# Kernel optimization log

Hardware: AMD Instinct MI355X
Metric: run time of the kernel (lower is better)

Reference implementation:

```python
import jax, jax.numpy as jnp
import numpy as np

N_STEP = 64
GAMMA = 10.0
DIST_MIN, DIST_MAX = 0.0, 10.0
N_LAYER = 4
H_DIM, E_DIM, HID_DIM = 128, 16, 256
N_NODES, N_EDGES = 10000, 320000


def setup_inputs() -> dict:
    key = jax.random.key(0)
    ks = jax.random.split(key, 12)
    in_m = 2 * H_DIM + E_DIM + N_STEP  # 336
    s = 0.02
    return {
        "x": jax.random.normal(ks[0], (N_NODES, H_DIM), jnp.float32),
        "pos": jax.random.normal(ks[1], (N_NODES, 3), jnp.float32),
        "edge_index": jax.random.randint(ks[2], (2, N_EDGES), 0, N_NODES),
        "edge_attr": jax.random.normal(ks[3], (N_EDGES, E_DIM), jnp.float32),
        "Wm": jax.random.normal(ks[4], (N_LAYER, in_m, HID_DIM), jnp.float32) * s,
        "bm": jnp.zeros((N_LAYER, HID_DIM), jnp.float32),
        "Wp": jax.random.normal(ks[5], (N_LAYER, HID_DIM, 1), jnp.float32) * s,
        "bp": jnp.zeros((N_LAYER, 1), jnp.float32),
        "Wx": jax.random.normal(ks[6], (N_LAYER, H_DIM + HID_DIM, H_DIM), jnp.float32) * s,
        "bx": jnp.zeros((N_LAYER, H_DIM), jnp.float32),
    }


def _egnn_layer(x, pos, edge_index, edge_attr, Wm, bm, Wp, bp, Wx, bx):
    i, j = edge_index[0], edge_index[1]
    n = x.shape[0]
    x_i, x_j = x[i], x[j]                       # [E, h] gathers
    # NOTE: source uses x (not pos) for the distance feature -- replicated.
    r = jnp.linalg.norm(x_i - x_j, axis=1)      # [E]
    c = jnp.linspace(DIST_MIN, DIST_MAX, N_STEP, dtype=x.dtype)
    soh = jnp.exp(-GAMMA * (r[:, None] - c[None, :]) ** 2)  # [E, n_step]
    m_ij = jnp.concatenate([x_i, x_j, soh, edge_attr], axis=1) @ Wm + bm  # [E, hid]
    _alpha = m_ij @ Wp + bp  # computed but unused in source's _update_pos
    # position update: scatter-mean of pos_i - pos_j over destination i
    pos_vect = pos[i] - pos[j]                  # [E, 3]
    cnt = jax.ops.segment_sum(jnp.ones((i.shape[0],), pos.dtype), i, num_segments=n)
    pos_aggr = jax.ops.segment_sum(pos_vect, i, num_segments=n) / jnp.maximum(cnt, 1.0)[:, None]
    pos = pos + pos_aggr
    # feature update: scatter-sum of messages
    m_aggr = jax.ops.segment_sum(m_ij, i, num_segments=n)  # [N, hid]
    x = jnp.concatenate([x, m_aggr], axis=1) @ Wx + bx      # [N, h]
    return x, pos


def reference(x, pos, edge_index, edge_attr, Wm, bm, Wp, bp, Wx, bx):
    x_ori = x
    for l in range(N_LAYER):
        x, pos = _egnn_layer(x, pos, edge_index, edge_attr,
                             Wm[l], bm[l], Wp[l], bp[l], Wx[l], bx[l])
        x = jax.nn.leaky_relu(x)
    x = x_ori + x            # residual_connection == 'add'
    x = jax.nn.leaky_relu(x)  # activate_last
    return x, pos
```

## Files before the change

### kernel.cpp

```cpp
#include <hip/hip_runtime.h>
#include <hip/hip_bf16.h>

#define NN 10000
#define NE 320000
#define HD 128
#define ED 16
#define HID 256
#define KP 480
#define AST 488
#define CAP 96
#define NBF 2161

typedef unsigned short ushort_t;
typedef long long i64;
typedef __attribute__((ext_vector_type(8))) short short8;
typedef __attribute__((ext_vector_type(4))) float f32x4;
typedef __attribute__((ext_vector_type(4))) unsigned int u32x4;

__device__ __forceinline__ float leaky(float v){ return v > 0.f ? v : 0.01f*v; }
__device__ __forceinline__ ushort_t f2bs(float v){
  __hip_bfloat16 b = __float2bfloat16(v);
  return *(ushort_t*)&b;
}
__device__ __forceinline__ unsigned pack2u(float a, float b){
  return (unsigned)f2bs(a) | ((unsigned)f2bs(b) << 16);
}
__device__ __forceinline__ float bl(unsigned u){ return __uint_as_float(u << 16); }
__device__ __forceinline__ float bh(unsigned u){ return __uint_as_float(u & 0xffff0000u); }
__device__ __forceinline__ float2 cvt2(unsigned u){ return make_float2(bl(u), bh(u)); }

__global__ __launch_bounds__(256) void k_misc(const float* __restrict__ x, ushort_t* __restrict__ xb,
                                              const int* __restrict__ ii, const int* __restrict__ jj,
                                              int* __restrict__ cnt, i64* __restrict__ sje,
                                              const float* __restrict__ Wx,
                                              const float* __restrict__ Wm, const float* __restrict__ bm,
                                              ushort_t* __restrict__ WcT){
  if (blockIdx.x < NBF){
    int t = blockIdx.x*256 + threadIdx.x;
    const int S1 = NE;
    const int S2 = NE + NN*HD/8;
    if (t < S1){
      int e = t;
      int a  = __builtin_nontemporal_load(ii + e);
      int jv = __builtin_nontemporal_load(jj + e);
      int r = atomicAdd(&cnt[a], 1);
      if (r < CAP)
        sje[(long)a*CAP + r] = ((i64)e << 32) | (unsigned)jv;
    } else if (t < S2){
      int u = t - S1;
      f32x4 a = __builtin_nontemporal_load(((const f32x4*)x) + 2*u);
      f32x4 b = __builtin_nontemporal_load(((const f32x4*)x) + 2*u + 1);
      u32x4 o;
      o.x = pack2u(a.x, a.y); o.y = pack2u(a.z, a.w);
      o.z = pack2u(b.x, b.y); o.w = pack2u(b.z, b.w);
      __builtin_nontemporal_store(o, ((u32x4*)xb) + u);
    } else if (t < S2 + 4*HD*HD){
      int u = t - S2;
      int l = u >> 14, r = (u >> 7) & 127, c = u & 127;
      float w = __builtin_nontemporal_load(Wx + (long)l*(HD+HID)*HD + r*HD + c);
      WcT[((long)l*HD + c)*KP + r] = f2bs(w);
    } else {
      int u = t - S2 - 4*HD*HD;
      if (u < 4*HD*15){
        int row = u / 15, k = 465 + u % 15;
        WcT[(long)row*KP + k] = 0;
      }
    }
    return;
  }
  __shared__ float a_s[16*36];
  __shared__ float w_s[16*128];
  int bi = blockIdx.x - NBF;
  int t  = threadIdx.x;
  int rb = (bi % 11) * 32;
  int l  = bi / 11;
  int lr = t >> 4, lk = t & 15;
  int wcc = t & 127, wk = t >> 7;
  int cg = t & 31, rg = t >> 5;
  const float* Wxb = Wx + (long)l*(HD+HID)*HD + HD*HD;
  float acc[4][4];
  #pragma unroll
  for (int i = 0; i < 4; ++i)
    #pragma unroll
    for (int j = 0; j < 4; ++j) acc[i][j] = 0.f;
  for (int k0 = 0; k0 < HID; k0 += 16){
    int m0 = rb + lr, m1 = rb + lr + 16;
    float v0 = 0.f, v1 = 0.f;
    if (m0 < 336) v0 = Wm[((long)l*336 + m0)*HID + k0 + lk];
    else if (m0 == 336) v0 = bm[l*HID + k0 + lk];
    if (m1 < 336) v1 = Wm[((long)l*336 + m1)*HID + k0 + lk];
    else if (m1 == 336) v1 = bm[l*HID + k0 + lk];
    a_s[lk*36 + lr]      = v0;
    a_s[lk*36 + lr + 16] = v1;
    #pragma unroll
    for (int q = 0; q < 8; ++q)
      w_s[(wk + 2*q)*128 + wcc] = Wxb[(k0 + wk + 2*q)*HD + wcc];
    __syncthreads();
    #pragma unroll
    for (int k = 0; k < 16; ++k){
      float4 av = *(const float4*)&a_s[k*36 + rg*4];
      float4 wv = *(const float4*)&w_s[k*128 + cg*4];
      acc[0][0] += av.x*wv.x; acc[0][1] += av.x*wv.y; acc[0][2] += av.x*wv.z; acc[0][3] += av.x*wv.w;
      acc[1][0] += av.y*wv.x; acc[1][1] += av.y*wv.y; acc[1][2] += av.y*wv.z; acc[1][3] += av.y*wv.w;
      acc[2][0] += av.z*wv.x; acc[2][1] += av.z*wv.y; acc[2][2] += av.z*wv.z; acc[2][3] += av.z*wv.w;
      acc[3][0] += av.w*wv.x; acc[3][1] += av.w*wv.y; acc[3][2] += av.w*wv.z; acc[3][3] += av.w*wv.w;
    }
    __syncthreads();
  }
  #pragma unroll
  for (int i = 0; i < 4; ++i){
    int m = rb + rg*4 + i;
    if (m < 337){
      #pragma unroll
      for (int j = 0; j < 4; ++j)
        WcT[((long)l*HD + cg*4 + j)*KP + 128 + m] = f2bs(acc[i][j]);
    }
  }
}

template<int FIRST, int FINAL>
__global__ __launch_bounds__(256) void k_layer(const uint4* __restrict__ xb4, const float* __restrict__ posf_cur,
                                               const int* __restrict__ cnt, const i64* __restrict__ sje,
                                               const float* __restrict__ ea,
                                               ushort_t* __restrict__ inv,
                                               const ushort_t* __restrict__ WcT, const float* __restrict__ bx,
                                               ushort_t* __restrict__ xb_next, const float* __restrict__ x_ori,
                                               float* __restrict__ out, float* __restrict__ posf_next){
  __shared__ ushort_t Asm[8*AST];
  __shared__ int sjL[8][64];
  __shared__ int seL[FIRST ? 8 : 1][64];
  int tid = threadIdx.x;
  int nl  = tid >> 5;
  int n   = blockIdx.x*8 + nl;
  int sub = tid & 31;
  int g   = sub >> 4;
  int gl  = sub & 15;
  int len = cnt[n];
  long beg = (long)n*CAP;
  int len2 = len < 64 ? len : 64;

  if (sub < len2){
    i64 lv = __builtin_nontemporal_load(sje + beg + sub);
    sjL[nl][sub] = (int)lv;
    if (FIRST) seL[nl][sub] = (int)(lv >> 32);
  }
  if (sub + 32 < len2){
    i64 lv = __builtin_nontemporal_load(sje + beg + sub + 32);
    sjL[nl][sub + 32] = (int)lv;
    if (FIRST) seL[nl][sub + 32] = (int)(lv >> 32);
  }
  __builtin_amdgcn_wave_barrier();

  uint4 xi = xb4[(long)n*16 + gl];
  float2 xi0 = cvt2(xi.x), xi1 = cvt2(xi.y), xi2 = cvt2(xi.z), xi3 = cvt2(xi.w);
  float c0 = (10.0f/63.0f)*(float)(4*gl);
  float c1 = (10.0f/63.0f)*(float)(4*gl+1);
  float c2 = (10.0f/63.0f)*(float)(4*gl+2);
  float c3 = (10.0f/63.0f)*(float)(4*gl+3);

  float2 s0 = {0,0}, s1 = {0,0}, s2 = {0,0}, s3 = {0,0};
  float h0 = 0, h1 = 0, h2 = 0, h3 = 0, sp = 0, sea = 0;
  int ec = gl & 3;
  int es = gl >> 2;

#define DPART(Bv, P) { \
    float2 e0=cvt2(Bv.x), e1=cvt2(Bv.y), e2=cvt2(Bv.z), e3=cvt2(Bv.w); \
    float d, q=0.f; \
    d=xi0.x-e0.x; q+=d*d;  d=xi0.y-e0.y; q+=d*d; \
    d=xi1.x-e1.x; q+=d*d;  d=xi1.y-e1.y; q+=d*d; \
    d=xi2.x-e2.x; q+=d*d;  d=xi2.y-e2.y; q+=d*d; \
    d=xi3.x-e3.x; q+=d*d;  d=xi3.y-e3.y; q+=d*d; \
    s0.x+=e0.x; s0.y+=e0.y; s1.x+=e1.x; s1.y+=e1.y; \
    s2.x+=e2.x; s2.y+=e2.y; s3.x+=e3.x; s3.y+=e3.y; \
    P = q; }

#define HPART(P) { \
    float r = sqrtf(P); \
    float t0=r-c0, t1=r-c1, t2=r-c2, t3=r-c3; \
    h0 += __expf(-10.f*t0*t0); h1 += __expf(-10.f*t1*t1); \
    h2 += __expf(-10.f*t2*t2); h3 += __expf(-10.f*t3*t3); }

#define LOADB(Bx, jx, ex, wv, off) { \
    jx[0]=sjL[nl][(off)]; jx[1]=sjL[nl][(off)+1]; jx[2]=sjL[nl][(off)+2]; jx[3]=sjL[nl][(off)+3]; \
    if (FIRST){ ex[0]=seL[nl][(off)]; ex[1]=seL[nl][(off)+1]; ex[2]=seL[nl][(off)+2]; ex[3]=seL[nl][(off)+3]; } \
    Bx[0] = xb4[(long)jx[0]*16 + gl]; \
    Bx[1] = xb4[(long)jx[1]*16 + gl]; \
    Bx[2] = xb4[(long)jx[2]*16 + gl]; \
    Bx[3] = xb4[(long)jx[3]*16 + gl]; \
    int jsel = (es==0) ? jx[0] : (es==1) ? jx[1] : (es==2) ? jx[2] : jx[3]; \
    wv = 0.f; \
    if (ec < 3) wv = posf_cur[(long)jsel*3 + ec]; }

#define COMPUTE(Bx, jx, ex, wv) { \
    float y0=0,y1=0,y2=0,y3=0; \
    if (FIRST){ \
      y0 = __builtin_nontemporal_load(ea + (long)ex[0]*ED + gl); \
      y1 = __builtin_nontemporal_load(ea + (long)ex[1]*ED + gl); \
      y2 = __builtin_nontemporal_load(ea + (long)ex[2]*ED + gl); \
      y3 = __builtin_nontemporal_load(ea + (long)ex[3]*ED + gl); } \
    float p0_,p1_,p2_,p3_; \
    DPART(Bx[0], p0_) DPART(Bx[1], p1_) DPART(Bx[2], p2_) DPART(Bx[3], p3_) \
    p0_ += __shfl_xor(p0_,1,64); p1_ += __shfl_xor(p1_,1,64); p2_ += __shfl_xor(p2_,1,64); p3_ += __shfl_xor(p3_,1,64); \
    p0_ += __shfl_xor(p0_,2,64); p1_ += __shfl_xor(p1_,2,64); p2_ += __shfl_xor(p2_,2,64); p3_ += __shfl_xor(p3_,2,64); \
    p0_ += __shfl_xor(p0_,4,64); p1_ += __shfl_xor(p1_,4,64); p2_ += __shfl_xor(p2_,4,64); p3_ += __shfl_xor(p3_,4,64); \
    p0_ += __shfl_xor(p0_,8,64); p1_ += __shfl_xor(p1_,8,64); p2_ += __shfl_xor(p2_,8,64); p3_ += __shfl_xor(p3_,8,64); \
    HPART(p0_) HPART(p1_) HPART(p2_) HPART(p3_) \
    sp += wv; \
    if (FIRST) sea += (y0+y1)+(y2+y3); }

#define EP1(Jv, Ev) { \
    uint4 Bv = xb4[(long)(Jv)*16 + gl]; \
    float wv1 = 0; if (gl < 3) wv1 = posf_cur[(long)(Jv)*3 + gl]; \
    float yv = 0; if (FIRST) yv = __builtin_nontemporal_load(ea + (long)(Ev)*ED + gl); \
    float pv; DPART(Bv, pv) \
    pv += __shfl_xor(pv,1,64); pv += __shfl_xor(pv,2,64); \
    pv += __shfl_xor(pv,4,64); pv += __shfl_xor(pv,8,64); \
    HPART(pv) \
    sp += wv1; if (FIRST) sea += yv; }

  int lo   = g ? (len2 >> 1) : 0;
  int hi   = g ? len2 : (len2 >> 1);
  int cntg = hi - lo;
  int nb4  = cntg >> 2;

  uint4 BA[4], BB_[4];
  int jA[4], jB[4], eA[4], eB[4];
  float wA, wB;
  (void)eA; (void)eB;
  if (nb4 > 0){
    LOADB(BA, jA, eA, wA, lo)
    int b = 1;
    for (; b + 1 < nb4; b += 2){
      LOADB(BB_, jB, eB, wB, lo + 4*b)
      COMPUTE(BA, jA, eA, wA)
      LOADB(BA, jA, eA, wA, lo + 4*b + 4)
      COMPUTE(BB_, jB, eB, wB)
    }
    if (b < nb4){
      LOADB(BB_, jB, eB, wB, lo + 4*b)
      COMPUTE(BA, jA, eA, wA)
      COMPUTE(BB_, jB, eB, wB)
    } else {
      COMPUTE(BA, jA, eA, wA)
    }
  }
  for (int k = lo + (nb4 << 2); k < hi; ++k){
    int jv = sjL[nl][k];
    int ev = FIRST ? seL[nl][k] : 0;
    EP1(jv, ev)
  }
  for (int q2 = 64 + g; q2 < len; q2 += 2){
    i64 lv = sje[beg + q2];
    int jv = (int)lv;
    int ev = FIRST ? (int)(lv >> 32) : 0;
    EP1(jv, ev)
  }
#undef DPART
#undef HPART
#undef LOADB
#undef COMPUTE
#undef EP1

  sp += __shfl_xor(sp,4,64); sp += __shfl_xor(sp,8,64);

  s0.x += __shfl_xor(s0.x,16,64); s0.y += __shfl_xor(s0.y,16,64);
  s1.x += __shfl_xor(s1.x,16,64); s1.y += __shfl_xor(s1.y,16,64);
  s2.x += __shfl_xor(s2.x,16,64); s2.y += __shfl_xor(s2.y,16,64);
  s3.x += __shfl_xor(s3.x,16,64); s3.y += __shfl_xor(s3.y,16,64);
  h0 += __shfl_xor(h0,16,64); h1 += __shfl_xor(h1,16,64);
  h2 += __shfl_xor(h2,16,64); h3 += __shfl_xor(h3,16,64);
  sp += __shfl_xor(sp,16,64);
  if (FIRST) sea += __shfl_xor(sea,16,64);

  if (g == 0){
    float cf = (float)len;
    ushort_t* Ar = Asm + nl*AST;
    ((uint4*)Ar)[gl] = xi;
    ((uint4*)(Ar + 128))[gl] = make_uint4(pack2u(cf*xi0.x, cf*xi0.y), pack2u(cf*xi1.x, cf*xi1.y),
                                          pack2u(cf*xi2.x, cf*xi2.y), pack2u(cf*xi3.x, cf*xi3.y));
    ((uint4*)(Ar + 256))[gl] = make_uint4(pack2u(s0.x, s0.y), pack2u(s1.x, s1.y),
                                          pack2u(s2.x, s2.y), pack2u(s3.x, s3.y));
    ((uint2*)(Ar + 384))[gl] = make_uint2(pack2u(h0, h1), pack2u(h2, h3));
    ushort_t sea_us;
    if (FIRST){
      sea_us = f2bs(sea);
      __builtin_nontemporal_store(sea_us, inv + (long)n*16 + gl);
    } else {
      sea_us = __builtin_nontemporal_load(inv + (long)n*16 + gl);
    }
    Ar[448 + gl] = sea_us;
    Ar[464 + gl] = (gl == 0) ? f2bs(cf) : (ushort_t)0;
    if (gl < 3){
      float pi = posf_cur[n*3 + gl];
      posf_next[n*3 + gl] = pi + (cf*pi - sp) / fmaxf(cf, 1.f);
    }
  }
  __syncthreads();

  int wave = tid >> 6, lane = tid & 63;
  int quad = lane >> 4, l16 = lane & 15;
  int nb = wave * 32;
  const ushort_t* Arow = Asm + (l16 & 7)*AST + quad*8;
  const ushort_t* W0 = WcT + (long)(nb + l16)*KP + quad*8;
  const ushort_t* W1 = WcT + (long)(nb + 16 + l16)*KP + quad*8;
  f32x4 acc0 = {0,0,0,0}, acc1 = {0,0,0,0};
  for (int k0 = 0; k0 < KP; k0 += 32){
    short8 av = *(const short8*)(Arow + k0);
    short8 b0 = *(const short8*)(W0 + k0);
    short8 b1 = *(const short8*)(W1 + k0);
    acc0 = __builtin_amdgcn_mfma_f32_16x16x32_bf16(av, b0, acc0, 0, 0, 0);
    acc1 = __builtin_amdgcn_mfma_f32_16x16x32_bf16(av, b1, acc1, 0, 0, 0);
  }
  float bx0 = bx[nb + l16], bx1 = bx[nb + 16 + l16];
  #pragma unroll
  for (int r = 0; r < 4; ++r){
    int row = quad*4 + r;
    if (row < 8){
      long base = (long)(blockIdx.x*8 + row)*HD;
      float v0 = leaky(acc0[r] + bx0);
      float v1 = leaky(acc1[r] + bx1);
      if (FINAL){
        float o0 = __builtin_nontemporal_load(x_ori + base + nb + l16);
        float o1 = __builtin_nontemporal_load(x_ori + base + nb + 16 + l16);
        __builtin_nontemporal_store(leaky(o0 + v0), out + base + nb + l16);
        __builtin_nontemporal_store(leaky(o1 + v1), out + base + nb + 16 + l16);
      } else {
        __builtin_nontemporal_store(f2bs(v0), xb_next + base + nb + l16);
        __builtin_nontemporal_store(f2bs(v1), xb_next + base + nb + 16 + l16);
      }
    }
  }
}

extern "C" void kernel_launch(void* const* d_in, const int* in_sizes, int n_in,
                              void* d_out, int out_size, void* d_ws, size_t ws_size,
                              hipStream_t stream){
  const float* x   = (const float*)d_in[0];
  const float* pos = (const float*)d_in[1];
  const int*   ei  = (const int*)d_in[2];
  const float* ea  = (const float*)d_in[3];
  const float* Wm  = (const float*)d_in[4];
  const float* bm  = (const float*)d_in[5];
  const float* Wx  = (const float*)d_in[8];
  const float* bx  = (const float*)d_in[9];
  float* out_x   = (float*)d_out;
  float* out_pos = out_x + NN*HD;

  ushort_t* xbA = (ushort_t*)d_ws;
  ushort_t* xbB = xbA + NN*HD;
  ushort_t* WcT = xbB + NN*HD;
  ushort_t* inv = WcT + 4*HD*KP;
  float*    pfA = (float*)(inv + NN*16);
  float*    pfB = pfA + NN*3;
  int*      cnt = (int*)(pfB + NN*3);
  i64*      sje = (i64*)(cnt + NN);
  const int* ii = ei;
  const int* jj = ei + NE;

  hipMemsetAsync(cnt, 0, NN*sizeof(int), stream);
  k_misc<<<NBF + 44, 256, 0, stream>>>(x, xbA, ii, jj, cnt, sje, Wx, Wm, bm, WcT);

  const float* ps[4] = {pos, pfA, pfB, pfA};
  float*       pd[4] = {pfA, pfB, pfA, out_pos};

  k_layer<1,0><<<1250, 256, 0, stream>>>((const uint4*)xbA, ps[0], cnt, sje, ea, inv,
                                         WcT + 0*HD*KP, bx + 0*HD, xbB, x, out_x, pd[0]);
  k_layer<0,0><<<1250, 256, 0, stream>>>((const uint4*)xbB, ps[1], cnt, sje, ea, inv,
                                         WcT + 1*(long)HD*KP, bx + 1*HD, xbA, x, out_x, pd[1]);
  k_layer<0,0><<<1250, 256, 0, stream>>>((const uint4*)xbA, ps[2], cnt, sje, ea, inv,
                                         WcT + 2*(long)HD*KP, bx + 2*HD, xbB, x, out_x, pd[2]);
  k_layer<0,1><<<1250, 256, 0, stream>>>((const uint4*)xbB, ps[3], cnt, sje, ea, inv,
                                         WcT + 3*(long)HD*KP, bx + 3*HD, xbA, x, out_x, pd[3]);
}
```

Baseline: 278.1 us.

## Stage combined weight matrix through LDS in K-chunked layout with register prefetch

Changes the WcT layout to K-chunks of 32 (chunk-major, column, k) so each 32-wide slab is contiguous. Each layer block then loads a slab cooperatively into an LDS buffer with a padded stride and prefetches the next slab into registers while the MFMAs read the current one. This replaces strided per-lane global weight reads with coalesced loads. It adds two block barriers per K step and extra LDS traffic. WcT is indexed without a layer offset in k_layer, so it relies on the caller passing a per-layer pointer.

After: 287.5 us. 1.03x slower.

```diff
diff --git a/kernel.cpp b/kernel.cpp
--- a/kernel.cpp
+++ b/kernel.cpp
@@ -10,6 +10,8 @@
 #define AST 488
 #define CAP 96
 #define NBF 2161
+#define WCH 4096
+#define WST 40
 
 typedef unsigned short ushort_t;
 typedef long long i64;
@@ -58,12 +60,12 @@
       int u = t - S2;
       int l = u >> 14, r = (u >> 7) & 127, c = u & 127;
       float w = __builtin_nontemporal_load(Wx + (long)l*(HD+HID)*HD + r*HD + c);
-      WcT[((long)l*HD + c)*KP + r] = f2bs(w);
+      WcT[(long)l*HD*KP + ((r>>5)*HD + c)*32 + (r&31)] = f2bs(w);
     } else {
       int u = t - S2 - 4*HD*HD;
       if (u < 4*HD*15){
         int row = u / 15, k = 465 + u % 15;
-        WcT[(long)row*KP + k] = 0;
+        WcT[(long)(row>>7)*HD*KP + (14*HD + (row&127))*32 + (k&31)] = 0;
       }
     }
     return;
@@ -111,9 +113,10 @@
   for (int i = 0; i < 4; ++i){
     int m = rb + rg*4 + i;
     if (m < 337){
+      int kg = 128 + m;
       #pragma unroll
       for (int j = 0; j < 4; ++j)
-        WcT[((long)l*HD + cg*4 + j)*KP + 128 + m] = f2bs(acc[i][j]);
+        WcT[(long)l*HD*KP + ((kg>>5)*HD + cg*4 + j)*32 + (kg&31)] = f2bs(acc[i][j]);
     }
   }
 }
@@ -129,6 +132,7 @@
   __shared__ ushort_t Asm[8*AST];
   __shared__ int sjL[8][64];
   __shared__ int seL[FIRST ? 8 : 1][64];
+  __shared__ ushort_t WL[128*WST];
   int tid = threadIdx.x;
   int nl  = tid >> 5;
   int n   = blockIdx.x*8 + nl;
@@ -138,6 +142,12 @@
   int len = cnt[n];
   long beg = (long)n*CAP;
   int len2 = len < 64 ? len : 64;
+
+  int scol = tid >> 1, spart = tid & 1;
+  int ssrc = scol*32 + spart*16;
+  int sdst = scol*WST + spart*16;
+  uint4 wr0 = *(const uint4*)(WcT + ssrc);
+  uint4 wr1 = *(const uint4*)(WcT + ssrc + 8);
 
   if (sub < len2){
     i64 lv = __builtin_nontemporal_load(sje + beg + sub);
@@ -301,13 +311,21 @@
   int quad = lane >> 4, l16 = lane & 15;
   int nb = wave * 32;
   const ushort_t* Arow = Asm + (l16 & 7)*AST + quad*8;
-  const ushort_t* W0 = WcT + (long)(nb + l16)*KP + quad*8;
-  const ushort_t* W1 = WcT + (long)(nb + 16 + l16)*KP + quad*8;
+  const ushort_t* rd0 = WL + (nb + l16)*WST + quad*8;
+  const ushort_t* rd1 = WL + (nb + 16 + l16)*WST + quad*8;
   f32x4 acc0 = {0,0,0,0}, acc1 = {0,0,0,0};
-  for (int k0 = 0; k0 < KP; k0 += 32){
-    short8 av = *(const short8*)(Arow + k0);
-    short8 b0 = *(const short8*)(W0 + k0);
-    short8 b1 = *(const short8*)(W1 + k0);
+  for (int c = 0; c < 15; ++c){
+    __syncthreads();
+    *(uint4*)(WL + sdst)     = wr0;
+    *(uint4*)(WL + sdst + 8) = wr1;
+    if (c + 1 < 15){
+      wr0 = *(const uint4*)(WcT + (c+1)*WCH + ssrc);
+      wr1 = *(const uint4*)(WcT + (c+1)*WCH + ssrc + 8);
+    }
+    __syncthreads();
+    short8 av = *(const short8*)(Arow + c*32);
+    short8 b0 = *(const short8*)(rd0);
+    short8 b1 = *(const short8*)(rd1);
     acc0 = __builtin_amdgcn_mfma_f32_16x16x32_bf16(av, b0, acc0, 0, 0, 0);
     acc1 = __builtin_amdgcn_mfma_f32_16x16x32_bf16(av, b1, acc1, 0, 0, 0);
   }
```
